# Performance work log

Measured on AMD Instinct MI355X. Metric: run time of the kernel, lower is better.

Reference implementation:

```python
import jax, jax.numpy as jnp
import numpy as np


def setup_inputs() -> dict:
    key = jax.random.key(0)
    kx, kw, kt, ks, kd, km = jax.random.split(key, 6)
    B, N, E, H, D = 1, 100000, 3200000, 8, 64
    X = jax.random.normal(kx, (B, N, H, D), dtype=jnp.float32)
    # glorot_uniform-like init for [D, H, 1]
    limit = (6.0 / (D + H)) ** 0.5
    attn_kernel = jax.random.uniform(kw, (D, H, 1), dtype=jnp.float32, minval=-limit, maxval=limit)
    targets = jax.random.randint(kt, (B, E), 0, N)
    sources = jax.random.randint(ks, (B, E), 0, N)
    degree = jax.random.uniform(kd, (B, N), dtype=jnp.float32)
    # tf.nn.dropout(x, 0.5): keep w.p. 0.5, scale kept by 1/0.5 = 2
    drop_mask = (jax.random.uniform(km, (B, E, H)) < 0.5).astype(jnp.float32) * 2.0
    return {"X": X, "attn_kernel": attn_kernel, "targets": targets,
            "sources": sources, "degree": degree, "drop_mask": drop_mask, "N": N}


def reference(X, attn_kernel, targets, sources, degree, drop_mask, N):
    # X: [B, N, H, D]; attn_kernel: [D, H, 1]; targets/sources: [B, E]
    B, _, H, D = X.shape
    E = targets.shape[1]
    W = attn_kernel[:, :, 0]                          # [D, H]
    attn = jnp.einsum('bnhd,dh->bnh', X, W)           # per-node scalar per head
    # gather to edges (tf.gather batch_dims=1): [B, E, H]
    e = jnp.take_along_axis(attn, sources[..., None], axis=1)
    e = jnp.tanh(e)
    # TF unsorted_segment_max with rank-2 ids pools over (batch, edge) jointly
    ids = targets.reshape(B * E)
    ef = e.reshape(B * E, H)
    m = jax.ops.segment_max(ef, ids, num_segments=N)  # [N, H]
    ef = jnp.exp(ef - m[ids])
    s = jax.ops.segment_max(ef, ids, num_segments=N) + 1e-9  # NOTE: max, not sum (faithful)
    ef = ef / s[ids]
    out = ef.reshape(B, E, H) * drop_mask
    return out[..., None]                             # [B, E, H, 1]
```

## Files before the change

kernel.cpp:

```cpp
#include <hip/hip_runtime.h>
#include <stdint.h>

#define HD 8
#define DD 64
#define BSHIFT 9
#define BRANGE 512
#define NBMAX 256

typedef float  vf4 __attribute__((ext_vector_type(4)));

__device__ __forceinline__ unsigned fmap(float f) {
    unsigned u = __float_as_uint(f);
    return u ^ (unsigned)(((int)u >> 31) | 0x80000000);
}
__device__ __forceinline__ float funmap(unsigned u) {
    u ^= ((int)u < 0) ? 0x80000000u : 0xFFFFFFFFu;
    return __uint_as_float(u);
}
#define FMAP_NEG_INF 0x007FFFFFu

__device__ __forceinline__ unsigned pack_bf16_rne(float a, float b) {
    unsigned ua = __float_as_uint(a); ua += 0x7FFF + ((ua >> 16) & 1);
    unsigned ub = __float_as_uint(b); ub += 0x7FFF + ((ub >> 16) & 1);
    return (ua >> 16) | (ub & 0xFFFF0000u);
}
__device__ __forceinline__ float bf_lo(unsigned u) { return __uint_as_float(u << 16); }
__device__ __forceinline__ float bf_hi(unsigned u) { return __uint_as_float(u & 0xFFFF0000u); }

__global__ __launch_bounds__(256) void attn_tanh_kernel(
    const float* __restrict__ X, const float* __restrict__ Wk,
    unsigned* __restrict__ t_pk, uint2* __restrict__ m_init,
    unsigned* __restrict__ gcnt, int NB, int N)
{
    __shared__ float Ws[DD * HD];
    int tid = threadIdx.x;
    for (int i = tid; i < DD * HD; i += 256) Ws[i] = Wk[i];

    int gid = blockIdx.x * 256 + tid;
    if (gcnt != nullptr && gid < NB) gcnt[gid] = 0;

    __syncthreads();

    int wave = tid >> 6, lane = tid & 63;
    int n0 = (blockIdx.x * 4 + wave) * 2;
    if (n0 >= N) return;
    bool two = (n0 + 1 < N);

    const vf4* Xa = (const vf4*)X + (size_t)n0 * 128;
    vf4 z = {0.f, 0.f, 0.f, 0.f};
    vf4 xv0 = Xa[lane];
    vf4 xv1 = Xa[64 + lane];
    vf4 xv2 = two ? Xa[128 + lane] : z;
    vf4 xv3 = two ? Xa[192 + lane] : z;

    int h0 = lane >> 4, d0 = (lane & 15) << 2;
    int h1 = 4 + h0;
    float w00 = Ws[(d0 + 0) * HD + h0], w01 = Ws[(d0 + 1) * HD + h0],
          w02 = Ws[(d0 + 2) * HD + h0], w03 = Ws[(d0 + 3) * HD + h0];
    float w10 = Ws[(d0 + 0) * HD + h1], w11 = Ws[(d0 + 1) * HD + h1],
          w12 = Ws[(d0 + 2) * HD + h1], w13 = Ws[(d0 + 3) * HD + h1];

    float p0 = xv0.x * w00 + xv0.y * w01 + xv0.z * w02 + xv0.w * w03;
    float p1 = xv1.x * w10 + xv1.y * w11 + xv1.z * w12 + xv1.w * w13;
    float p2 = xv2.x * w00 + xv2.y * w01 + xv2.z * w02 + xv2.w * w03;
    float p3 = xv3.x * w10 + xv3.y * w11 + xv3.z * w12 + xv3.w * w13;

    for (int off = 8; off; off >>= 1) {
        p0 += __shfl_xor(p0, off);
        p1 += __shfl_xor(p1, off);
        p2 += __shfl_xor(p2, off);
        p3 += __shfl_xor(p3, off);
    }
    if ((lane & 15) == 0) {
        int g = lane >> 4;
        t_pk[(size_t)n0 * 4 + g] = pack_bf16_rne(tanhf(p0), tanhf(p1));
        m_init[(size_t)n0 * 4 + g] = make_uint2(FMAP_NEG_INF, FMAP_NEG_INF);
        if (two) {
            t_pk[(size_t)(n0 + 1) * 4 + g] = pack_bf16_rne(tanhf(p2), tanhf(p3));
            m_init[(size_t)(n0 + 1) * 4 + g] = make_uint2(FMAP_NEG_INF, FMAP_NEG_INF);
        }
    }
}

__global__ __launch_bounds__(256) void bin_kernel(
    const int* __restrict__ sources, const int* __restrict__ targets,
    unsigned* __restrict__ gcnt, unsigned* __restrict__ buf,
    const uint4* __restrict__ t_pk4, unsigned* __restrict__ m_u,
    int NB, int CAPB, int SRC_BITS, int E)
{
    __shared__ unsigned hist[NBMAX];
    __shared__ unsigned base[NBMAX];
    __shared__ unsigned cur[NBMAX];
    int tid = threadIdx.x;
    if (tid < NB) { hist[tid] = 0; cur[tid] = 0; }
    __syncthreads();

    int e0 = blockIdx.x * 4096;
    #pragma unroll
    for (int k = 0; k < 16; ++k) {
        int e = e0 + k * 256 + tid;
        if (e < E) {
            int tg = targets[e];
            atomicAdd(&hist[tg >> BSHIFT], 1u);
        }
    }
    __syncthreads();
    if (tid < NB && hist[tid] != 0)
        base[tid] = atomicAdd(gcnt + tid, hist[tid]);
    __syncthreads();

    #pragma unroll
    for (int k = 0; k < 16; ++k) {
        int e = e0 + k * 256 + tid;
        if (e < E) {
            int tg = targets[e];
            int s  = sources[e];
            int b  = tg >> BSHIFT;
            unsigned pos = base[b] + atomicAdd(&cur[b], 1u);
            if (pos < (unsigned)CAPB) {
                buf[(size_t)b * CAPB + pos] =
                    ((unsigned)(tg & (BRANGE - 1)) << SRC_BITS) | (unsigned)s;
            } else {
                uint4 tv = t_pk4[s];
                unsigned* mp = m_u + (size_t)tg * HD;
                atomicMax(mp + 0, fmap(bf_lo(tv.x)));
                atomicMax(mp + 1, fmap(bf_hi(tv.x)));
                atomicMax(mp + 2, fmap(bf_lo(tv.y)));
                atomicMax(mp + 3, fmap(bf_hi(tv.y)));
                atomicMax(mp + 4, fmap(bf_lo(tv.z)));
                atomicMax(mp + 5, fmap(bf_hi(tv.z)));
                atomicMax(mp + 6, fmap(bf_lo(tv.w)));
                atomicMax(mp + 7, fmap(bf_hi(tv.w)));
            }
        }
    }
}

__global__ __launch_bounds__(256) void reduce_kernel(
    const unsigned* __restrict__ gcnt, const unsigned* __restrict__ buf,
    const uint4* __restrict__ t_pk4, const unsigned* __restrict__ m_u,
    uint4* __restrict__ m_pk, int CAPB, int SRC_BITS, int N)
{
    __shared__ unsigned mt[BRANGE * HD];
    int tid = threadIdx.x;
    int b = blockIdx.x;
    for (int i = tid; i < BRANGE * HD; i += 256) mt[i] = FMAP_NEG_INF;
    __syncthreads();

    unsigned cnt = gcnt[b];
    if (cnt > (unsigned)CAPB) cnt = CAPB;
    unsigned srcmask = (1u << SRC_BITS) - 1;
    const unsigned* bb = buf + (size_t)b * CAPB;

    for (unsigned i = tid; i < cnt; i += 256) {
        unsigned rec = bb[i];
        unsigned s  = rec & srcmask;
        unsigned tl = rec >> SRC_BITS;
        uint4 tv = t_pk4[s];
        unsigned* mp = mt + tl * HD;
        atomicMax(mp + 0, fmap(bf_lo(tv.x)));
        atomicMax(mp + 1, fmap(bf_hi(tv.x)));
        atomicMax(mp + 2, fmap(bf_lo(tv.y)));
        atomicMax(mp + 3, fmap(bf_hi(tv.y)));
        atomicMax(mp + 4, fmap(bf_lo(tv.z)));
        atomicMax(mp + 5, fmap(bf_hi(tv.z)));
        atomicMax(mp + 6, fmap(bf_lo(tv.w)));
        atomicMax(mp + 7, fmap(bf_hi(tv.w)));
    }
    __syncthreads();

    int n0 = b << BSHIFT;
    for (int tl = tid; tl < BRANGE; tl += 256) {
        int n = n0 + tl;
        if (n < N) {
            const unsigned* ms = mt + tl * HD;
            const unsigned* mu = m_u + (size_t)n * HD;
            float v0 = fmaxf(funmap(ms[0]), funmap(mu[0]));
            float v1 = fmaxf(funmap(ms[1]), funmap(mu[1]));
            float v2 = fmaxf(funmap(ms[2]), funmap(mu[2]));
            float v3 = fmaxf(funmap(ms[3]), funmap(mu[3]));
            float v4 = fmaxf(funmap(ms[4]), funmap(mu[4]));
            float v5 = fmaxf(funmap(ms[5]), funmap(mu[5]));
            float v6 = fmaxf(funmap(ms[6]), funmap(mu[6]));
            float v7 = fmaxf(funmap(ms[7]), funmap(mu[7]));
            uint4 o;
            o.x = pack_bf16_rne(v0, v1);
            o.y = pack_bf16_rne(v2, v3);
            o.z = pack_bf16_rne(v4, v5);
            o.w = pack_bf16_rne(v6, v7);
            m_pk[n] = o;
        }
    }
}


__global__ __launch_bounds__(256) void seg_max_kernel(
    const int* __restrict__ sources, const int* __restrict__ targets,
    const uint4* __restrict__ t_pk4, unsigned* __restrict__ m_u, int E)
{
    int e = blockIdx.x * 256 + threadIdx.x;
    if (e >= E) return;
    int s  = __builtin_nontemporal_load(sources + e);
    int tg = __builtin_nontemporal_load(targets + e);
    uint4 tv = t_pk4[s];
    unsigned* mp = m_u + (size_t)tg * HD;
    const uint4* m4 = (const uint4*)mp;
    uint4 c0 = m4[0];
    uint4 c1 = m4[1];
    unsigned f;
    f = fmap(bf_lo(tv.x)); if (f > c0.x) atomicMax(mp + 0, f);
    f = fmap(bf_hi(tv.x)); if (f > c0.y) atomicMax(mp + 1, f);
    f = fmap(bf_lo(tv.y)); if (f > c0.z) atomicMax(mp + 2, f);
    f = fmap(bf_hi(tv.y)); if (f > c0.w) atomicMax(mp + 3, f);
    f = fmap(bf_lo(tv.z)); if (f > c1.x) atomicMax(mp + 4, f);
    f = fmap(bf_hi(tv.z)); if (f > c1.y) atomicMax(mp + 5, f);
    f = fmap(bf_lo(tv.w)); if (f > c1.z) atomicMax(mp + 6, f);
    f = fmap(bf_hi(tv.w)); if (f > c1.w) atomicMax(mp + 7, f);
}

__global__ __launch_bounds__(256) void pack_m_kernel(
    const unsigned* __restrict__ m_u, uint4* __restrict__ m_pk, int N)
{
    int n = blockIdx.x * 256 + threadIdx.x;
    if (n >= N) return;
    const uint4* mu4 = (const uint4*)m_u + (size_t)n * 2;
    uint4 c0 = mu4[0];
    uint4 c1 = mu4[1];
    uint4 o;
    o.x = (__float_as_uint(funmap(c0.x)) >> 16) | (__float_as_uint(funmap(c0.y)) & 0xFFFF0000u);
    o.y = (__float_as_uint(funmap(c0.z)) >> 16) | (__float_as_uint(funmap(c0.w)) & 0xFFFF0000u);
    o.z = (__float_as_uint(funmap(c1.x)) >> 16) | (__float_as_uint(funmap(c1.y)) & 0xFFFF0000u);
    o.w = (__float_as_uint(funmap(c1.z)) >> 16) | (__float_as_uint(funmap(c1.w)) & 0xFFFF0000u);
    m_pk[n] = o;
}

__global__ __launch_bounds__(256) void finalize_kernel(
    const int* __restrict__ sources, const int* __restrict__ targets,
    const uint4* __restrict__ t_pk4, const uint4* __restrict__ m_pk,
    const float* __restrict__ dm, float* __restrict__ out, int E)
{
    int e = blockIdx.x * 256 + threadIdx.x;
    if (e >= E) return;
    int s  = __builtin_nontemporal_load(sources + e);
    int tg = __builtin_nontemporal_load(targets + e);
    uint4 tv = t_pk4[s];
    uint4 mv = m_pk[tg];
    const vf4* dm4 = (const vf4*)dm;
    vf4 d0 = dm4[(size_t)e * 2];
    vf4 d1 = dm4[(size_t)e * 2 + 1];
    vf4 o0, o1;
    o0.x = expf(bf_lo(tv.x) - bf_lo(mv.x)) * d0.x;
    o0.y = expf(bf_lo(tv.y) - bf_lo(mv.y)) * d0.y;
    o0.z = expf(bf_lo(tv.z) - bf_lo(mv.z)) * d0.z;
    o0.w = expf(bf_lo(tv.w) - bf_lo(mv.w)) * d0.w;
    o1.x = expf(bf_hi(tv.x) - bf_hi(mv.x)) * d1.x;
    o1.y = expf(bf_hi(tv.y) - bf_hi(mv.y)) * d1.y;
    o1.z = expf(bf_hi(tv.z) - bf_hi(mv.z)) * d1.z;
    o1.w = expf(bf_hi(tv.w) - bf_hi(mv.w)) * d1.w;
    vf4* out4 = (vf4*)out;
    out4[(size_t)e * 2]     = o0;
    out4[(size_t)e * 2 + 1] = o1;
}

extern "C" void kernel_launch(void* const* d_in, const int* in_sizes, int n_in,
                              void* d_out, int out_size, void* d_ws, size_t ws_size,
                              hipStream_t stream)
{
    const float* X       = (const float*)d_in[0];
    const float* Wk      = (const float*)d_in[1];
    const int*   targets = (const int*)d_in[2];
    const int*   sources = (const int*)d_in[3];
    const float* dm      = (const float*)d_in[5];

    int E = in_sizes[2];
    int N = in_sizes[4];

    float* out = (float*)d_out;
    int blocksA = (N + 7) / 8;
    int blocksE = (E + 255) / 256;

    int NB = (N + BRANGE - 1) >> BSHIFT;
    int SRC_BITS = 1;
    while ((1 << SRC_BITS) < N && SRC_BITS < 31) ++SRC_BITS;
    bool packable = (NB <= NBMAX) && (SRC_BITS + BSHIFT <= 32);
    long long capll = ((long long)(E + NB - 1) / (NB > 0 ? NB : 1));
    capll = (capll * 3) / 2;
    capll = (capll + 255) & ~255LL;
    int CAPB = (int)capll;

    size_t needed = (size_t)N * 68 + (size_t)NB * (size_t)CAPB * 4;

    char* w = (char*)d_ws;
    unsigned* t_pk = (unsigned*)w;
    unsigned* m_u  = (unsigned*)(w + (size_t)N * 16);
    uint4*    m_pk = (uint4*)  (w + (size_t)N * 48);

    if (packable && ws_size >= needed) {
        unsigned* gcnt = (unsigned*)(w + (size_t)N * 64);
        unsigned* buf  = (unsigned*)(w + (size_t)N * 68);

        attn_tanh_kernel<<<blocksA, 256, 0, stream>>>(X, Wk, t_pk, (uint2*)m_u, gcnt, NB, N);
        int blocksB = (E + 4095) / 4096;
        bin_kernel<<<blocksB, 256, 0, stream>>>(sources, targets, gcnt, buf,
                                                (const uint4*)t_pk, m_u, NB, CAPB, SRC_BITS, E);
        reduce_kernel<<<NB, 256, 0, stream>>>(gcnt, buf, (const uint4*)t_pk, m_u,
                                              m_pk, CAPB, SRC_BITS, N);
        finalize_kernel<<<blocksE, 256, 0, stream>>>(sources, targets, (const uint4*)t_pk,
                                                     m_pk, dm, out, E);
    } else {
        attn_tanh_kernel<<<blocksA, 256, 0, stream>>>(X, Wk, t_pk, (uint2*)m_u, nullptr, 0, N);
        seg_max_kernel<<<blocksE, 256, 0, stream>>>(sources, targets, (const uint4*)t_pk, m_u, E);
        int blocksN = (N + 255) / 256;
        pack_m_kernel<<<blocksN, 256, 0, stream>>>(m_u, m_pk, N);
        finalize_kernel<<<blocksE, 256, 0, stream>>>(sources, targets, (const uint4*)t_pk,
                                                     m_pk, dm, out, E);
    }
}
```

Baseline: 530.5 us.

## Use per-wave bin histograms, smaller bins, padded reduce LDS, two-edge finalize

Halves the target bin width, replaces the single block histogram and cursor in binning with per-wave histograms plus prefix offsets, pads the shared max table to stride 9 with 512-thread reduce blocks, and makes finalize process two edges per thread with fast exp and nontemporal stores. These target shared-atomic contention, LDS bank conflicts, and per-thread memory-level parallelism in the bandwidth-bound output pass. Fast exp slightly changes numerics; more bins raise the bin count and buffer overhead.

```diff
diff --git a/kernel.cpp b/kernel.cpp
--- a/kernel.cpp
+++ b/kernel.cpp
@@ -3,9 +3,9 @@
 
 #define HD 8
 #define DD 64
-#define BSHIFT 9
-#define BRANGE 512
-#define NBMAX 256
+#define BSHIFT 8
+#define BRANGE 256
+#define NBMAX 512
 
 typedef float  vf4 __attribute__((ext_vector_type(4)));
 
@@ -88,25 +88,31 @@
     const uint4* __restrict__ t_pk4, unsigned* __restrict__ m_u,
     int NB, int CAPB, int SRC_BITS, int E)
 {
-    __shared__ unsigned hist[NBMAX];
-    __shared__ unsigned base[NBMAX];
-    __shared__ unsigned cur[NBMAX];
+    __shared__ unsigned whist[4][NBMAX];
     int tid = threadIdx.x;
-    if (tid < NB) { hist[tid] = 0; cur[tid] = 0; }
+    int wv  = tid >> 6;
+    for (int i = tid; i < 4 * NBMAX; i += 256) ((unsigned*)whist)[i] = 0;
     __syncthreads();
 
     int e0 = blockIdx.x * 4096;
     #pragma unroll
     for (int k = 0; k < 16; ++k) {
         int e = e0 + k * 256 + tid;
-        if (e < E) {
-            int tg = targets[e];
-            atomicAdd(&hist[tg >> BSHIFT], 1u);
+        if (e < E) atomicAdd(&whist[wv][targets[e] >> BSHIFT], 1u);
+    }
+    __syncthreads();
+
+    for (int i = tid; i < NB; i += 256) {
+        unsigned h0 = whist[0][i], h1 = whist[1][i], h2 = whist[2][i], h3 = whist[3][i];
+        unsigned tot = h0 + h1 + h2 + h3;
+        if (tot) {
+            unsigned g = atomicAdd(gcnt + i, tot);
+            whist[0][i] = g;
+            whist[1][i] = g + h0;
+            whist[2][i] = g + h0 + h1;
+            whist[3][i] = g + h0 + h1 + h2;
         }
     }
-    __syncthreads();
-    if (tid < NB && hist[tid] != 0)
-        base[tid] = atomicAdd(gcnt + tid, hist[tid]);
     __syncthreads();
 
     #pragma unroll
@@ -116,7 +122,7 @@
             int tg = targets[e];
             int s  = sources[e];
             int b  = tg >> BSHIFT;
-            unsigned pos = base[b] + atomicAdd(&cur[b], 1u);
+            unsigned pos = atomicAdd(&whist[wv][b], 1u);
             if (pos < (unsigned)CAPB) {
                 buf[(size_t)b * CAPB + pos] =
                     ((unsigned)(tg & (BRANGE - 1)) << SRC_BITS) | (unsigned)s;
@@ -136,15 +142,16 @@
     }
 }
 
-__global__ __launch_bounds__(256) void reduce_kernel(
+#define MTS 9
+__global__ __launch_bounds__(512) void reduce_kernel(
     const unsigned* __restrict__ gcnt, const unsigned* __restrict__ buf,
     const uint4* __restrict__ t_pk4, const unsigned* __restrict__ m_u,
     uint4* __restrict__ m_pk, int CAPB, int SRC_BITS, int N)
 {
-    __shared__ unsigned mt[BRANGE * HD];
+    __shared__ unsigned mt[BRANGE * MTS];
     int tid = threadIdx.x;
     int b = blockIdx.x;
-    for (int i = tid; i < BRANGE * HD; i += 256) mt[i] = FMAP_NEG_INF;
+    for (int i = tid; i < BRANGE * MTS; i += 512) mt[i] = FMAP_NEG_INF;
     __syncthreads();
 
     unsigned cnt = gcnt[b];
@@ -152,12 +159,12 @@
     unsigned srcmask = (1u << SRC_BITS) - 1;
     const unsigned* bb = buf + (size_t)b * CAPB;
 
-    for (unsigned i = tid; i < cnt; i += 256) {
+    for (unsigned i = tid; i < cnt; i += 512) {
         unsigned rec = bb[i];
         unsigned s  = rec & srcmask;
         unsigned tl = rec >> SRC_BITS;
         uint4 tv = t_pk4[s];
-        unsigned* mp = mt + tl * HD;
+        unsigned* mp = mt + tl * MTS;
         atomicMax(mp + 0, fmap(bf_lo(tv.x)));
         atomicMax(mp + 1, fmap(bf_hi(tv.x)));
         atomicMax(mp + 2, fmap(bf_lo(tv.y)));
@@ -170,10 +177,10 @@
     __syncthreads();
 
     int n0 = b << BSHIFT;
-    for (int tl = tid; tl < BRANGE; tl += 256) {
+    for (int tl = tid; tl < BRANGE; tl += 512) {
         int n = n0 + tl;
         if (n < N) {
-            const unsigned* ms = mt + tl * HD;
+            const unsigned* ms = mt + tl * MTS;
             const unsigned* mu = m_u + (size_t)n * HD;
             float v0 = fmaxf(funmap(ms[0]), funmap(mu[0]));
             float v1 = fmaxf(funmap(ms[1]), funmap(mu[1]));
@@ -239,27 +246,51 @@
     const uint4* __restrict__ t_pk4, const uint4* __restrict__ m_pk,
     const float* __restrict__ dm, float* __restrict__ out, int E)
 {
-    int e = blockIdx.x * 256 + threadIdx.x;
-    if (e >= E) return;
-    int s  = __builtin_nontemporal_load(sources + e);
-    int tg = __builtin_nontemporal_load(targets + e);
-    uint4 tv = t_pk4[s];
-    uint4 mv = m_pk[tg];
+    int e0 = (blockIdx.x * 256 + threadIdx.x) * 2;
+    if (e0 >= E) return;
+    bool two = (e0 + 1 < E);
+
+    int s0  = __builtin_nontemporal_load(sources + e0);
+    int tg0 = __builtin_nontemporal_load(targets + e0);
+    int s1  = two ? __builtin_nontemporal_load(sources + e0 + 1) : s0;
+    int tg1 = two ? __builtin_nontemporal_load(targets + e0 + 1) : tg0;
+
     const vf4* dm4 = (const vf4*)dm;
-    vf4 d0 = dm4[(size_t)e * 2];
-    vf4 d1 = dm4[(size_t)e * 2 + 1];
-    vf4 o0, o1;
-    o0.x = expf(bf_lo(tv.x) - bf_lo(mv.x)) * d0.x;
-    o0.y = expf(bf_lo(tv.y) - bf_lo(mv.y)) * d0.y;
-    o0.z = expf(bf_lo(tv.z) - bf_lo(mv.z)) * d0.z;
-    o0.w = expf(bf_lo(tv.w) - bf_lo(mv.w)) * d0.w;
-    o1.x = expf(bf_hi(tv.x) - bf_hi(mv.x)) * d1.x;
-    o1.y = expf(bf_hi(tv.y) - bf_hi(mv.y)) * d1.y;
-    o1.z = expf(bf_hi(tv.z) - bf_hi(mv.z)) * d1.z;
-    o1.w = expf(bf_hi(tv.w) - bf_hi(mv.w)) * d1.w;
+    vf4 a0 = dm4[(size_t)e0 * 2];
+    vf4 a1 = dm4[(size_t)e0 * 2 + 1];
+    vf4 b0 = two ? dm4[(size_t)e0 * 2 + 2] : a0;
+    vf4 b1 = two ? dm4[(size_t)e0 * 2 + 3] : a1;
+
+    uint4 tv0 = t_pk4[s0];
+    uint4 mv0 = m_pk[tg0];
+    uint4 tv1 = t_pk4[s1];
+    uint4 mv1 = m_pk[tg1];
+
+    vf4 o0, o1, o2, o3;
+    o0.x = __expf(bf_lo(tv0.x) - bf_lo(mv0.x)) * a0.x;
+    o0.y = __expf(bf_lo(tv0.y) - bf_lo(mv0.y)) * a0.y;
+    o0.z = __expf(bf_lo(tv0.z) - bf_lo(mv0.z)) * a0.z;
+    o0.w = __expf(bf_lo(tv0.w) - bf_lo(mv0.w)) * a0.w;
+    o1.x = __expf(bf_hi(tv0.x) - bf_hi(mv0.x)) * a1.x;
+    o1.y = __expf(bf_hi(tv0.y) - bf_hi(mv0.y)) * a1.y;
+    o1.z = __expf(bf_hi(tv0.z) - bf_hi(mv0.z)) * a1.z;
+    o1.w = __expf(bf_hi(tv0.w) - bf_hi(mv0.w)) * a1.w;
+    o2.x = __expf(bf_lo(tv1.x) - bf_lo(mv1.x)) * b0.x;
+    o2.y = __expf(bf_lo(tv1.y) - bf_lo(mv1.y)) * b0.y;
+    o2.z = __expf(bf_lo(tv1.z) - bf_lo(mv1.z)) * b0.z;
+    o2.w = __expf(bf_lo(tv1.w) - bf_lo(mv1.w)) * b0.w;
+    o3.x = __expf(bf_hi(tv1.x) - bf_hi(mv1.x)) * b1.x;
+    o3.y = __expf(bf_hi(tv1.y) - bf_hi(mv1.y)) * b1.y;
+    o3.z = __expf(bf_hi(tv1.z) - bf_hi(mv1.z)) * b1.z;
+    o3.w = __expf(bf_hi(tv1.w) - bf_hi(mv1.w)) * b1.w;
+
     vf4* out4 = (vf4*)out;
-    out4[(size_t)e * 2]     = o0;
-    out4[(size_t)e * 2 + 1] = o1;
+    __builtin_nontemporal_store(o0, out4 + (size_t)e0 * 2);
+    __builtin_nontemporal_store(o1, out4 + (size_t)e0 * 2 + 1);
+    if (two) {
+        __builtin_nontemporal_store(o2, out4 + (size_t)e0 * 2 + 2);
+        __builtin_nontemporal_store(o3, out4 + (size_t)e0 * 2 + 3);
+    }
 }
 
 extern "C" void kernel_launch(void* const* d_in, const int* in_sizes, int n_in,
@@ -277,7 +308,7 @@
 
     float* out = (float*)d_out;
     int blocksA = (N + 7) / 8;
-    int blocksE = (E + 255) / 256;
+    int blocksF = (E + 511) / 512;
 
     int NB = (N + BRANGE - 1) >> BSHIFT;
     int SRC_BITS = 1;
@@ -303,16 +334,17 @@
         int blocksB = (E + 4095) / 4096;
         bin_kernel<<<blocksB, 256, 0, stream>>>(sources, targets, gcnt, buf,
                                                 (const uint4*)t_pk, m_u, NB, CAPB, SRC_BITS, E);
-        reduce_kernel<<<NB, 256, 0, stream>>>(gcnt, buf, (const uint4*)t_pk, m_u,
+        reduce_kernel<<<NB, 512, 0, stream>>>(gcnt, buf, (const uint4*)t_pk, m_u,
                                               m_pk, CAPB, SRC_BITS, N);
-        finalize_kernel<<<blocksE, 256, 0, stream>>>(sources, targets, (const uint4*)t_pk,
+        finalize_kernel<<<blocksF, 256, 0, stream>>>(sources, targets, (const uint4*)t_pk,
                                                      m_pk, dm, out, E);
     } else {
         attn_tanh_kernel<<<blocksA, 256, 0, stream>>>(X, Wk, t_pk, (uint2*)m_u, nullptr, 0, N);
+        int blocksE = (E + 255) / 256;
         seg_max_kernel<<<blocksE, 256, 0, stream>>>(sources, targets, (const uint4*)t_pk, m_u, E);
         int blocksN = (N + 255) / 256;
         pack_m_kernel<<<blocksN, 256, 0, stream>>>(m_u, m_pk, N);
-        finalize_kernel<<<blocksE, 256, 0, stream>>>(sources, targets, (const uint4*)t_pk,
+        finalize_kernel<<<blocksF, 256, 0, stream>>>(sources, targets, (const uint4*)t_pk,
                                                      m_pk, dm, out, E);
     }
 }
```

After: 569.6 us. +7.4%, slower.
